# Kernel tuning notes

Hardware: AMD Instinct MI355X
Metric: run time of the kernel (lower is better)

Reference implementation:

```python
import jax, jax.numpy as jnp
import numpy as np
from jax.scipy.linalg import expm

HIDDEN = 1024
STATE = 64
INTER = 4096
EPS = 1e-06
DT_MIN, DT_MAX = 0.001, 0.1


def rmsnorm(x, w, eps=EPS):
    var = jnp.mean(x * x, axis=-1, keepdims=True)
    return x * jax.lax.rsqrt(var + eps) * w


def setup_inputs() -> dict:
    key = jax.random.key(0)
    ks = jax.random.split(key, 10)
    hidden_states = jax.random.normal(ks[0], (4, 2048, HIDDEN), dtype=jnp.float32)
    A = jax.random.normal(ks[1], (STATE, STATE), dtype=jnp.float32) * 0.01
    B = jax.random.normal(ks[2], (STATE, HIDDEN), dtype=jnp.float32) * 0.01
    C = jax.random.normal(ks[3], (HIDDEN, STATE), dtype=jnp.float32) * 0.01
    D = jnp.ones((HIDDEN,), dtype=jnp.float32)
    log_dt = jax.random.uniform(ks[4], (HIDDEN,), dtype=jnp.float32) * (np.log(DT_MAX) - np.log(DT_MIN)) + np.log(DT_MIN)
    s = 1.0 / np.sqrt(HIDDEN)
    w_gate = jax.random.uniform(ks[5], (INTER, HIDDEN), minval=-s, maxval=s, dtype=jnp.float32)
    w_up = jax.random.uniform(ks[6], (INTER, HIDDEN), minval=-s, maxval=s, dtype=jnp.float32)
    s2 = 1.0 / np.sqrt(INTER)
    w_down = jax.random.uniform(ks[7], (HIDDEN, INTER), minval=-s2, maxval=s2, dtype=jnp.float32)
    ln1_w = jnp.ones((HIDDEN,), dtype=jnp.float32)
    ln2_w = jnp.ones((HIDDEN,), dtype=jnp.float32)
    return {"hidden_states": hidden_states, "A": A, "B": B, "C": C, "D": D,
            "log_dt": log_dt, "w_gate": w_gate, "w_up": w_up, "w_down": w_down,
            "ln1_w": ln1_w, "ln2_w": ln2_w}


def ssm(x, A, B, C, D, log_dt):
    # x: (batch, seq, hidden)
    dt = jnp.exp(log_dt)                    # (hidden,)
    A_bar = expm(A * jnp.mean(dt))          # (state, state)
    B_bar = B * dt[None, :]                 # (state, hidden)

    def step(state, x_t):
        # state: (batch, state); x_t: (batch, hidden)
        state = state @ A_bar.T + x_t @ B_bar.T
        out = state @ C.T + D * x_t
        return state, out

    x_t = jnp.swapaxes(x, 0, 1)             # (seq, batch, hidden)
    init = jnp.zeros((x.shape[0], A.shape[0]), dtype=x.dtype)
    _, ys = jax.lax.scan(step, init, x_t)
    return jnp.swapaxes(ys, 0, 1)           # (batch, seq, hidden)


def reference(hidden_states, A, B, C, D, log_dt, w_gate, w_up, w_down, ln1_w, ln2_w):
    # pre-norm SSM mixer + residual
    residual = hidden_states
    h = rmsnorm(hidden_states, ln1_w)
    h = ssm(h, A, B, C, D, log_dt)
    h = residual + h
    # pre-norm SwiGLU FFN + residual
    residual = h
    hn = rmsnorm(h, ln2_w)
    gate = hn @ w_gate.T
    up = hn @ w_up.T
    ffn = (jax.nn.silu(gate) * up) @ w_down.T
    return residual + ffn
```

## Files before the change

kernel.cpp:

```cpp
#include <hip/hip_runtime.h>
#include <hip/hip_bf16.h>
#include <math.h>

typedef __attribute__((ext_vector_type(8))) short short8;
typedef __attribute__((ext_vector_type(4))) float f32x4;
typedef __attribute__((ext_vector_type(4))) int int4v;
typedef __attribute__((ext_vector_type(8))) int int8v;

__device__ __forceinline__ unsigned short f2b(float x) {
  union { float f; unsigned int u; } v; v.f = x;
  unsigned int r = v.u + 0x7fffu + ((v.u >> 16) & 1u);
  return (unsigned short)(r >> 16);
}
__device__ __forceinline__ float b2f(unsigned short u) {
  union { unsigned int u; float f; } v; v.u = ((unsigned int)u) << 16;
  return v.f;
}
__device__ __forceinline__ unsigned char f2f8_sw(float x) {
  float a = fabsf(x);
  unsigned char s = (x < 0.f) ? 0x80 : 0x00;
  if (a >= 464.f) return s | 0x7E;
  union { float f; unsigned u; } v; v.f = a;
  int e = (int)(v.u >> 23) - 127;
  if (e < -6) {
    int q = (int)rintf(a * 512.f);
    if (q >= 8) return s | 0x08;
    return s | (unsigned char)q;
  }
  unsigned mant = v.u & 0x7FFFFF;
  unsigned keep = mant >> 20;
  unsigned rest = mant & 0xFFFFF;
  if (rest > 0x80000u || (rest == 0x80000u && (keep & 1))) keep++;
  unsigned exp8 = (unsigned)(e + 7);
  if (keep == 8) { keep = 0; exp8++; }
  if (exp8 >= 15 && keep >= 7) return s | 0x7E;
  return s | (unsigned char)((exp8 << 3) | keep);
}
#if __has_builtin(__builtin_amdgcn_cvt_pk_fp8_f32)
__device__ __forceinline__ unsigned char f2f8(float x) {
  return (unsigned char)(__builtin_amdgcn_cvt_pk_fp8_f32(x, x, 0, false) & 0xFF);
}
__device__ __forceinline__ unsigned int f8pack4(float a, float b, float c, float d) {
  int w0 = __builtin_amdgcn_cvt_pk_fp8_f32(a, b, 0, false);
  return (unsigned int)__builtin_amdgcn_cvt_pk_fp8_f32(c, d, w0, true);
}
#else
__device__ __forceinline__ unsigned char f2f8(float x) { return f2f8_sw(x); }
__device__ __forceinline__ unsigned int f8pack4(float a, float b, float c, float d) {
  return (unsigned)f2f8_sw(a) | ((unsigned)f2f8_sw(b) << 8) |
         ((unsigned)f2f8_sw(c) << 16) | ((unsigned)f2f8_sw(d) << 24);
}
#endif
__device__ __forceinline__ void async_ld16(const void* g, void* l) {
  __builtin_amdgcn_global_load_lds(
      (const __attribute__((address_space(1))) void*)g,
      (__attribute__((address_space(3))) void*)l, 16, 0, 0);
}

__device__ __forceinline__ f32x4 mx_fp8(int4v alo, int4v ahi, int4v blo, int4v bhi, f32x4 c) {
#if __has_builtin(__builtin_amdgcn_mfma_scale_f32_16x16x128_f8f6f4)
  int8v a = __builtin_shufflevector(alo, ahi, 0, 1, 2, 3, 4, 5, 6, 7);
  int8v b = __builtin_shufflevector(blo, bhi, 0, 1, 2, 3, 4, 5, 6, 7);
  return __builtin_amdgcn_mfma_scale_f32_16x16x128_f8f6f4(
      a, b, c, 0, 0, 0, 0x7F7F7F7F, 0, 0x7F7F7F7F);
#else
  int4v av[2] = {alo, ahi}, bv[2] = {blo, bhi};
  const long* al = (const long*)av;
  const long* bl = (const long*)bv;
#pragma unroll
  for (int j = 0; j < 4; j++)
    c = __builtin_amdgcn_mfma_f32_16x16x32_fp8_fp8(al[j], bl[j], c, 0, 0, 0);
  return c;
#endif
}

__global__ __launch_bounds__(1024) void prep_combo(
    const float* __restrict__ A, const float* __restrict__ logdt,
    float* __restrict__ Abar, float* __restrict__ A64,
    const float* __restrict__ B, const float* __restrict__ Cm,
    unsigned short* __restrict__ Bb, unsigned short* __restrict__ Cb) {
  __shared__ float red[16];
  __shared__ float Ms[4096], T[4096], P[4096];
  if (blockIdx.x != 0) {
    const size_t NB = 65536, NC = 65536;
    size_t base = (size_t)(blockIdx.x - 1) * 1024 + threadIdx.x;
    size_t stride = (size_t)(gridDim.x - 1) * 1024;
    for (size_t id = base; id < NB + NC; id += stride) {
      if (id < NB) { int k = (int)(id & 1023); Bb[id] = f2b(B[id] * expf(logdt[k])); }
      else Cb[id - NB] = f2b(Cm[id - NB]);
    }
    return;
  }
  const int tid = threadIdx.x;
  const int c = tid & 63;
  const int w = tid >> 6;
  float e = expf(logdt[tid]);
#pragma unroll
  for (int off = 32; off > 0; off >>= 1) e += __shfl_down(e, off);
  if (c == 0) red[w] = e;
  __syncthreads();
  if (tid == 0) {
    float s = 0.f;
    for (int i = 0; i < 16; i++) s += red[i];
    red[0] = s * (1.f / 1024.f);
  }
  __syncthreads();
  const float mdt = red[0];
  {
    float m0 = A[tid] * mdt, m1 = A[tid + 1024] * mdt,
          m2 = A[tid + 2048] * mdt, m3 = A[tid + 3072] * mdt;
    Ms[tid] = m0; Ms[tid + 1024] = m1; Ms[tid + 2048] = m2; Ms[tid + 3072] = m3;
    T[tid] = m0; T[tid + 1024] = m1; T[tid + 2048] = m2; T[tid + 3072] = m3;
    P[tid] = m0 + ((tid >> 6) == (tid & 63) ? 1.f : 0.f);
    P[tid + 1024] = m1 + (((tid + 1024) >> 6) == ((tid + 1024) & 63) ? 1.f : 0.f);
    P[tid + 2048] = m2 + (((tid + 2048) >> 6) == ((tid + 2048) & 63) ? 1.f : 0.f);
    P[tid + 3072] = m3 + (((tid + 3072) >> 6) == ((tid + 3072) & 63) ? 1.f : 0.f);
  }
  __syncthreads();
  float colM[64];
#pragma unroll
  for (int j = 0; j < 64; j++) colM[j] = Ms[j * 64 + c];
  for (int k = 2; k <= 6; k++) {
    const float inv = 1.f / (float)k;
    float accs[4];
#pragma unroll
    for (int i = 0; i < 4; i++) {
      const int r = w + 16 * i;
      const float4* Trow = (const float4*)(T + r * 64);
      float a0 = 0.f, a1 = 0.f, a2 = 0.f, a3 = 0.f;
#pragma unroll
      for (int j4 = 0; j4 < 16; j4++) {
        const float4 t = Trow[j4];
        a0 += t.x * colM[4 * j4 + 0]; a1 += t.y * colM[4 * j4 + 1];
        a2 += t.z * colM[4 * j4 + 2]; a3 += t.w * colM[4 * j4 + 3];
      }
      accs[i] = ((a0 + a1) + (a2 + a3)) * inv;
    }
    __syncthreads();
#pragma unroll
    for (int i = 0; i < 4; i++) {
      const int r = w + 16 * i;
      T[r * 64 + c] = accs[i];
      P[r * 64 + c] += accs[i];
    }
    __syncthreads();
  }
#pragma unroll
  for (int i = 0; i < 4; i++) {
    const int r = w + 16 * i;
    Abar[r * 64 + c] = P[r * 64 + c];
    T[r * 64 + c] = P[r * 64 + c];
  }
  __syncthreads();
  for (int sq = 0; sq < 6; sq++) {
    float colT[64];
#pragma unroll
    for (int j = 0; j < 64; j++) colT[j] = T[j * 64 + c];
    float accs[4];
#pragma unroll
    for (int i = 0; i < 4; i++) {
      const int r = w + 16 * i;
      const float4* Trow = (const float4*)(T + r * 64);
      float a0 = 0.f, a1 = 0.f, a2 = 0.f, a3 = 0.f;
#pragma unroll
      for (int j4 = 0; j4 < 16; j4++) {
        const float4 t = Trow[j4];
        a0 += t.x * colT[4 * j4 + 0]; a1 += t.y * colT[4 * j4 + 1];
        a2 += t.z * colT[4 * j4 + 2]; a3 += t.w * colT[4 * j4 + 3];
      }
      accs[i] = (a0 + a1) + (a2 + a3);
    }
    __syncthreads();
#pragma unroll
    for (int i = 0; i < 4; i++) T[(w + 16 * i) * 64 + c] = accs[i];
    __syncthreads();
  }
#pragma unroll
  for (int i = 0; i < 4; i++) {
    const int r = w + 16 * i;
    A64[r * 64 + c] = T[r * 64 + c];
  }
}

__global__ __launch_bounds__(256) void rmsnorm_bf16(
    const float* __restrict__ x, const float* __restrict__ w,
    unsigned short* __restrict__ out) {
  const size_t row = blockIdx.x;
  const int tid = threadIdx.x;
  const float4 v = ((const float4*)(x + row * 1024))[tid];
  float ss = v.x * v.x + v.y * v.y + v.z * v.z + v.w * v.w;
#pragma unroll
  for (int off = 32; off > 0; off >>= 1) ss += __shfl_down(ss, off);
  __shared__ float wsum[4];
  if ((tid & 63) == 0) wsum[tid >> 6] = ss;
  __syncthreads();
  const float tot = wsum[0] + wsum[1] + wsum[2] + wsum[3];
  const float rs = rsqrtf(tot * (1.f / 1024.f) + 1e-6f);
  const float4 wv = ((const float4*)w)[tid];
  ushort4 o;
  o.x = f2b(v.x * rs * wv.x); o.y = f2b(v.y * rs * wv.y);
  o.z = f2b(v.z * rs * wv.z); o.w = f2b(v.w * rs * wv.w);
  ((ushort4*)(out + row * 1024))[tid] = o;
}

__global__ __launch_bounds__(256) void rmsnorm_f8(
    const float* __restrict__ x, const float* __restrict__ w,
    unsigned int* __restrict__ out) {
  const size_t row = blockIdx.x;
  const int tid = threadIdx.x;
  const float4 v = ((const float4*)(x + row * 1024))[tid];
  float ss = v.x * v.x + v.y * v.y + v.z * v.z + v.w * v.w;
#pragma unroll
  for (int off = 32; off > 0; off >>= 1) ss += __shfl_down(ss, off);
  __shared__ float wsum[4];
  if ((tid & 63) == 0) wsum[tid >> 6] = ss;
  __syncthreads();
  const float tot = wsum[0] + wsum[1] + wsum[2] + wsum[3];
  const float rs = rsqrtf(tot * (1.f / 1024.f) + 1e-6f);
  const float4 wv = ((const float4*)w)[tid];
  out[row * 256 + tid] =
      f8pack4(v.x * rs * wv.x, v.y * rs * wv.y, v.z * rs * wv.z, v.w * rs * wv.w);
}

template <int STORE_S>
__global__ __launch_bounds__(256) void scan_combo(
    const float* __restrict__ U, const float* __restrict__ Abar,
    const float* __restrict__ carry, float* __restrict__ zend,
    unsigned short* __restrict__ S,
    const float* __restrict__ csrc, unsigned char* __restrict__ cdst, size_t ccount) {
  constexpr int SCAN_BLOCKS = 32;
  __shared__ float s[4][64];
  if (blockIdx.x >= SCAN_BLOCKS) {
    size_t base = (size_t)(blockIdx.x - SCAN_BLOCKS) * 256 + threadIdx.x;
    size_t stride = (size_t)(gridDim.x - SCAN_BLOCKS) * 256;
    for (size_t id = base; id < ccount; id += stride)
      cdst[id] = f2f8(csrc[id] * 64.f);
    return;
  }
  const int wave = threadIdx.x >> 6, i = threadIdx.x & 63;
  const int task = blockIdx.x * 4 + wave;
  const int b = task >> 5, c = task & 31;
  float a[64];
#pragma unroll
  for (int j = 0; j < 64; j++) a[j] = Abar[i * 64 + j];
  float cur = STORE_S ? carry[(b * 32 + c) * 64 + i] : 0.f;
  const float* Ub = U + ((size_t)(b * 2048 + c * 64)) * 64;
  for (int t = 0; t < 64; t++) {
    s[wave][i] = cur;
    __syncthreads();
    const float u = Ub[t * 64 + i];
    const float4* s4 = (const float4*)s[wave];
    float a0 = u, a1 = 0.f, a2 = 0.f, a3 = 0.f;
#pragma unroll
    for (int j = 0; j < 16; j++) {
      float4 v = s4[j];
      a0 += a[4 * j + 0] * v.x; a1 += a[4 * j + 1] * v.y;
      a2 += a[4 * j + 2] * v.z; a3 += a[4 * j + 3] * v.w;
    }
    cur = (a0 + a1) + (a2 + a3);
    __syncthreads();
    if (STORE_S) S[((size_t)(b * 2048 + c * 64 + t)) * 64 + i] = f2b(cur);
  }
  if (!STORE_S) zend[(b * 32 + c) * 64 + i] = cur;
}

__global__ __launch_bounds__(256) void carry_combo(
    const float* __restrict__ zend, const float* __restrict__ A64,
    float* __restrict__ carry,
    const float* __restrict__ csrc, unsigned char* __restrict__ cdst, size_t ccount) {
  __shared__ float s[4][64];
  if (blockIdx.x != 0) {
    size_t base = (size_t)(blockIdx.x - 1) * 256 + threadIdx.x;
    size_t stride = (size_t)(gridDim.x - 1) * 256;
    for (size_t id = base; id < ccount; id += stride)
      cdst[id] = f2f8(csrc[id] * 64.f);
    return;
  }
  const int b = threadIdx.x >> 6, i = threadIdx.x & 63;
  float a[64];
#pragma unroll
  for (int j = 0; j < 64; j++) a[j] = A64[i * 64 + j];
  float cur = 0.f;
  for (int c = 0; c < 32; c++) {
    carry[(b * 32 + c) * 64 + i] = cur;
    s[b][i] = cur;
    __syncthreads();
    const float z = zend[(b * 32 + c) * 64 + i];
    const float4* s4 = (const float4*)s[b];
    float a0 = z, a1 = 0.f, a2 = 0.f, a3 = 0.f;
#pragma unroll
    for (int j = 0; j < 16; j++) {
      float4 v = s4[j];
      a0 += a[4 * j + 0] * v.x; a1 += a[4 * j + 1] * v.y;
      a2 += a[4 * j + 2] * v.z; a3 += a[4 * j + 3] * v.w;
    }
    cur = (a0 + a1) + (a2 + a3);
    __syncthreads();
  }
}

template <int BM, int BN, int WAVES_M, int WAVES_N, int EPI>
__global__ void __launch_bounds__(256) gemm_bt(
    const unsigned short* __restrict__ X, const unsigned short* __restrict__ W,
    int M, int N, int K,
    float* __restrict__ outf, const unsigned short* __restrict__ e_b,
    const float* __restrict__ e_f, const float* __restrict__ e_d) {
  constexpr int BK = 64;
  constexpr int SM = BM / WAVES_M, SN = BN / WAVES_N;
  constexpr int TM = SM / 16, TN = SN / 16;
  __shared__ unsigned short aT[BM * BK];
  __shared__ unsigned short bT[BN * BK];
  const int tid = threadIdx.x;
  const int lane = tid & 63, wave = tid >> 6;
  const int wm = wave / WAVES_N, wn = wave % WAVES_N;
  const int lm = lane & 15, quad = lane >> 4;
  const long bm0 = (long)blockIdx.y * BM;
  const long bn0 = (long)blockIdx.x * BN;
  const int wb = tid & ~63;

  f32x4 acc[TM][TN];
#pragma unroll
  for (int i = 0; i < TM; i++)
#pragma unroll
    for (int j = 0; j < TN; j++) acc[i][j] = (f32x4){0.f, 0.f, 0.f, 0.f};

  for (int k0 = 0; k0 < K; k0 += BK) {
#pragma unroll
    for (int it = 0; it < (BM * 8) / 256; ++it) {
      int slot = it * 256 + tid;
      int r = slot >> 3, cp = slot & 7, c = cp ^ (r & 7);
      async_ld16(X + (bm0 + r) * (long)K + k0 + c * 8, aT + (it * 256 + wb) * 8);
    }
#pragma unroll
    for (int it = 0; it < (BN * 8) / 256; ++it) {
      int slot = it * 256 + tid;
      int r = slot >> 3, cp = slot & 7, c = cp ^ (r & 7);
      async_ld16(W + (bn0 + r) * (long)K + k0 + c * 8, bT + (it * 256 + wb) * 8);
    }
    __syncthreads();
#pragma unroll
    for (int kk = 0; kk < BK; kk += 32) {
      const int cch = (kk >> 3) + quad;
      short8 af[TM], bf[TN];
#pragma unroll
      for (int i = 0; i < TM; i++) {
        int r = wm * SM + i * 16 + lm;
        af[i] = *(const short8*)(aT + (r * 8 + (cch ^ (r & 7))) * 8);
      }
#pragma unroll
      for (int j = 0; j < TN; j++) {
        int r = wn * SN + j * 16 + lm;
        bf[j] = *(const short8*)(bT + (r * 8 + (cch ^ (r & 7))) * 8);
      }
#pragma unroll
      for (int i = 0; i < TM; i++)
#pragma unroll
        for (int j = 0; j < TN; j++)
          acc[i][j] = __builtin_amdgcn_mfma_f32_16x16x32_bf16(af[i], bf[j], acc[i][j], 0, 0, 0);
    }
    __syncthreads();
  }
#pragma unroll
  for (int i = 0; i < TM; i++) {
#pragma unroll
    for (int j = 0; j < TN; j++) {
#pragma unroll
      for (int r = 0; r < 4; r++) {
        const long m = bm0 + wm * SM + i * 16 + quad * 4 + r;
        const long n = bn0 + wn * SN + j * 16 + lm;
        const long idx = m * N + n;
        const float v = acc[i][j][r];
        if (EPI == 0) outf[idx] = v;
        else if (EPI == 4) outf[idx] = v + e_d[n] * b2f(e_b[idx]) + e_f[idx];
      }
    }
  }
}

__global__ void __launch_bounds__(256) gemm_gu(
    const unsigned char* __restrict__ X, const unsigned char* __restrict__ Wg,
    const unsigned char* __restrict__ Wu, int M, int N, int K,
    unsigned char* __restrict__ out8, float inv) {
  constexpr int BM = 128, BN = 64, BK = 128;
  constexpr int TM = 4, TN = 2;
  __shared__ __attribute__((aligned(16))) unsigned char aT[BM * BK];
  __shared__ __attribute__((aligned(16))) unsigned char gT[BN * BK];
  __shared__ __attribute__((aligned(16))) unsigned char uT[BN * BK];
  const int tid = threadIdx.x;
  const int lane = tid & 63, wave = tid >> 6;
  const int wm = wave >> 1, wn = wave & 1;
  const int lm = lane & 15, quad = lane >> 4;
  const long bm0 = (long)blockIdx.y * BM;
  const long bn0 = (long)blockIdx.x * BN;
  const int wb = tid & ~63;

  f32x4 accg[TM][TN], accu[TM][TN];
#pragma unroll
  for (int i = 0; i < TM; i++)
#pragma unroll
    for (int j = 0; j < TN; j++) {
      accg[i][j] = (f32x4){0.f, 0.f, 0.f, 0.f};
      accu[i][j] = (f32x4){0.f, 0.f, 0.f, 0.f};
    }

  for (int k0 = 0; k0 < K; k0 += BK) {
#pragma unroll
    for (int it = 0; it < 4; ++it) {
      int slot = it * 256 + tid;
      int r = slot >> 3, cp = slot & 7, c = cp ^ (r & 7);
      async_ld16(X + (bm0 + r) * (long)K + k0 + c * 16, aT + (it * 256 + wb) * 16);
    }
#pragma unroll
    for (int it = 0; it < 2; ++it) {
      int slot = it * 256 + tid;
      int r = slot >> 3, cp = slot & 7, c = cp ^ (r & 7);
      async_ld16(Wg + (bn0 + r) * (long)K + k0 + c * 16, gT + (it * 256 + wb) * 16);
    }
#pragma unroll
    for (int it = 0; it < 2; ++it) {
      int slot = it * 256 + tid;
      int r = slot >> 3, cp = slot & 7, c = cp ^ (r & 7);
      async_ld16(Wu + (bn0 + r) * (long)K + k0 + c * 16, uT + (it * 256 + wb) * 16);
    }
    __syncthreads();
    int4v alo[TM], ahi[TM], glo[TN], ghi[TN], ulo[TN], uhi[TN];
#pragma unroll
    for (int i = 0; i < TM; i++) {
      int r = wm * 64 + i * 16 + lm;
      alo[i] = *(const int4v*)(aT + (r * 8 + ((2 * quad) ^ (r & 7))) * 16);
      ahi[i] = *(const int4v*)(aT + (r * 8 + ((2 * quad + 1) ^ (r & 7))) * 16);
    }
#pragma unroll
    for (int j = 0; j < TN; j++) {
      int r = wn * 32 + j * 16 + lm;
      glo[j] = *(const int4v*)(gT + (r * 8 + ((2 * quad) ^ (r & 7))) * 16);
      ghi[j] = *(const int4v*)(gT + (r * 8 + ((2 * quad + 1) ^ (r & 7))) * 16);
      ulo[j] = *(const int4v*)(uT + (r * 8 + ((2 * quad) ^ (r & 7))) * 16);
      uhi[j] = *(const int4v*)(uT + (r * 8 + ((2 * quad + 1) ^ (r & 7))) * 16);
    }
#pragma unroll
    for (int i = 0; i < TM; i++)
#pragma unroll
      for (int j = 0; j < TN; j++) {
        accg[i][j] = mx_fp8(alo[i], ahi[i], glo[j], ghi[j], accg[i][j]);
        accu[i][j] = mx_fp8(alo[i], ahi[i], ulo[j], uhi[j], accu[i][j]);
      }
    __syncthreads();
  }
#pragma unroll
  for (int i = 0; i < TM; i++) {
#pragma unroll
    for (int j = 0; j < TN; j++) {
#pragma unroll
      for (int r = 0; r < 4; r++) {
        const long m = bm0 + wm * 64 + i * 16 + quad * 4 + r;
        const long n = bn0 + wn * 32 + j * 16 + lm;
        const float g = accg[i][j][r] * inv;
        const float u = accu[i][j][r] * inv;
        const float s = g / (1.f + __expf(-g));
        out8[m * N + n] = f2f8(s * u);
      }
    }
  }
}

__global__ void __launch_bounds__(256) gemm_f8(
    const unsigned char* __restrict__ X, const unsigned char* __restrict__ W,
    int M, int N, int K,
    float* __restrict__ outf, const float* __restrict__ e_f, float inv) {
  constexpr int BM = 128, BN = 64, BK = 128;
  constexpr int TM = 4, TN = 2;
  __shared__ __attribute__((aligned(16))) unsigned char aT[BM * BK];
  __shared__ __attribute__((aligned(16))) unsigned char bT[BN * BK];
  const int tid = threadIdx.x;
  const int lane = tid & 63, wave = tid >> 6;
  const int wm = wave >> 1, wn = wave & 1;
  const int lm = lane & 15, quad = lane >> 4;
  const long bm0 = (long)blockIdx.y * BM;
  const long bn0 = (long)blockIdx.x * BN;
  const int wb = tid & ~63;

  f32x4 acc[TM][TN];
#pragma unroll
  for (int i = 0; i < TM; i++)
#pragma unroll
    for (int j = 0; j < TN; j++) acc[i][j] = (f32x4){0.f, 0.f, 0.f, 0.f};

  for (int k0 = 0; k0 < K; k0 += BK) {
#pragma unroll
    for (int it = 0; it < 4; ++it) {
      int slot = it * 256 + tid;
      int r = slot >> 3, cp = slot & 7, c = cp ^ (r & 7);
      async_ld16(X + (bm0 + r) * (long)K + k0 + c * 16, aT + (it * 256 + wb) * 16);
    }
#pragma unroll
    for (int it = 0; it < 2; ++it) {
      int slot = it * 256 + tid;
      int r = slot >> 3, cp = slot & 7, c = cp ^ (r & 7);
      async_ld16(W + (bn0 + r) * (long)K + k0 + c * 16, bT + (it * 256 + wb) * 16);
    }
    __syncthreads();
    int4v alo[TM], ahi[TM], blo[TN], bhi[TN];
#pragma unroll
    for (int i = 0; i < TM; i++) {
      int r = wm * 64 + i * 16 + lm;
      alo[i] = *(const int4v*)(aT + (r * 8 + ((2 * quad) ^ (r & 7))) * 16);
      ahi[i] = *(const int4v*)(aT + (r * 8 + ((2 * quad + 1) ^ (r & 7))) * 16);
    }
#pragma unroll
    for (int j = 0; j < TN; j++) {
      int r = wn * 32 + j * 16 + lm;
      blo[j] = *(const int4v*)(bT + (r * 8 + ((2 * quad) ^ (r & 7))) * 16);
      bhi[j] = *(const int4v*)(bT + (r * 8 + ((2 * quad + 1) ^ (r & 7))) * 16);
    }
#pragma unroll
    for (int i = 0; i < TM; i++)
#pragma unroll
      for (int j = 0; j < TN; j++)
        acc[i][j] = mx_fp8(alo[i], ahi[i], blo[j], bhi[j], acc[i][j]);
    __syncthreads();
  }
#pragma unroll
  for (int i = 0; i < TM; i++) {
#pragma unroll
    for (int j = 0; j < TN; j++) {
#pragma unroll
      for (int r = 0; r < 4; r++) {
        const long m = bm0 + wm * 64 + i * 16 + quad * 4 + r;
        const long n = bn0 + wn * 32 + j * 16 + lm;
        const long idx = m * N + n;
        outf[idx] = acc[i][j][r] * inv + e_f[idx];
      }
    }
  }
}

extern "C" void kernel_launch(void* const* d_in, const int* in_sizes, int n_in,
                              void* d_out, int out_size, void* d_ws, size_t ws_size,
                              hipStream_t stream) {
  const float* x     = (const float*)d_in[0];
  const float* A     = (const float*)d_in[1];
  const float* B     = (const float*)d_in[2];
  const float* C     = (const float*)d_in[3];
  const float* D     = (const float*)d_in[4];
  const float* logdt = (const float*)d_in[5];
  const float* wg    = (const float*)d_in[6];
  const float* wu    = (const float*)d_in[7];
  const float* wd    = (const float*)d_in[8];
  const float* ln1   = (const float*)d_in[9];
  const float* ln2   = (const float*)d_in[10];
  float* out = (float*)d_out;

  char* p = (char*)d_ws;
  auto alloc = [&](size_t bytes) { char* q = p; p += (bytes + 255) & ~(size_t)255; return q; };
  float* Abar  = (float*)alloc(64 * 64 * 4);
  float* A64   = (float*)alloc(64 * 64 * 4);
  float* zend  = (float*)alloc(4 * 32 * 64 * 4);
  float* carry = (float*)alloc(4 * 32 * 64 * 4);
  float* U     = (float*)alloc((size_t)8192 * 64 * 4);
  unsigned short* S    = (unsigned short*)alloc((size_t)8192 * 64 * 2);
  unsigned short* Bb   = (unsigned short*)alloc((size_t)64 * 1024 * 2);
  unsigned short* Cb   = (unsigned short*)alloc((size_t)1024 * 64 * 2);
  unsigned char*  wg8  = (unsigned char*)alloc((size_t)4096 * 1024);
  unsigned char*  wu8  = (unsigned char*)alloc((size_t)4096 * 1024);
  unsigned char*  wd8  = (unsigned char*)alloc((size_t)1024 * 4096);
  unsigned short* xnb  = (unsigned short*)alloc((size_t)8192 * 1024 * 2);
  unsigned char*  hn8  = (unsigned char*)alloc((size_t)8192 * 1024);
  float* h             = (float*)alloc((size_t)8192 * 1024 * 4);
  unsigned char*  act8 = (unsigned char*)alloc((size_t)8192 * 4096);

  const size_t NWG = (size_t)4096 * 1024;

  prep_combo<<<33, 1024, 0, stream>>>(A, logdt, Abar, A64, B, C, Bb, Cb);
  rmsnorm_bf16<<<8192, 256, 0, stream>>>(x, ln1, xnb);
  gemm_bt<32, 64, 2, 2, 0><<<dim3(1, 256), 256, 0, stream>>>(
      xnb, Bb, 8192, 64, 1024, U, nullptr, nullptr, nullptr);
  scan_combo<0><<<32 + 1024, 256, 0, stream>>>(
      U, Abar, nullptr, zend, S, wg, wg8, NWG);
  carry_combo<<<1 + 1024, 256, 0, stream>>>(zend, A64, carry, wu, wu8, NWG);
  scan_combo<1><<<32 + 1024, 256, 0, stream>>>(
      U, Abar, carry, zend, S, wd, wd8, NWG);
  gemm_bt<128, 128, 2, 2, 4><<<dim3(8, 64), 256, 0, stream>>>(
      S, Cb, 8192, 1024, 64, h, xnb, x, D);
  rmsnorm_f8<<<8192, 256, 0, stream>>>(h, ln2, (unsigned int*)hn8);
  gemm_gu<<<dim3(64, 64), 256, 0, stream>>>(
      hn8, wg8, wu8, 8192, 4096, 1024, act8, 1.f / 64.f);
  gemm_f8<<<dim3(16, 64), 256, 0, stream>>>(
      act8, wd8, 8192, 1024, 4096, out, h, 1.f / 64.f);
}
```

Measured before the change: 430.1 us.

## Triple-buffer FP8 FFN GEMMs with async loads and larger 512-thread tiles

Rewrites the gate/up and down-projection FP8 GEMMs to use 512-thread blocks with 256-row tiles (and 128-column tiles for the down projection). The main loop keeps three dynamic-LDS stages, issues async global-to-LDS loads two steps ahead, and waits with explicit vmcnt and raw barriers instead of __syncthreads. LDS reads now fetch 32-byte fragments with a new swizzle, and MFMA issue is wrapped in setprio. The aim is to hide global load latency and raise data reuse per block. The cost is 144KB of LDS per block and fewer blocks, which may limit occupancy or fill the GPU unevenly.

Result: slower. 447.8 us (+4.1%).

```diff
diff --git a/kernel.cpp b/kernel.cpp
--- a/kernel.cpp
+++ b/kernel.cpp
@@ -57,19 +57,19 @@
       (__attribute__((address_space(3))) void*)l, 16, 0, 0);
 }
 
-__device__ __forceinline__ f32x4 mx_fp8(int4v alo, int4v ahi, int4v blo, int4v bhi, f32x4 c) {
+#define VMCNT6()  asm volatile("s_waitcnt vmcnt(6)" ::: "memory")
+#define VMCNT0()  asm volatile("s_waitcnt vmcnt(0)" ::: "memory")
+#define LGKM0()   asm volatile("s_waitcnt lgkmcnt(0)" ::: "memory")
+
+__device__ __forceinline__ f32x4 mx8(int8v a, int8v b, f32x4 c) {
 #if __has_builtin(__builtin_amdgcn_mfma_scale_f32_16x16x128_f8f6f4)
-  int8v a = __builtin_shufflevector(alo, ahi, 0, 1, 2, 3, 4, 5, 6, 7);
-  int8v b = __builtin_shufflevector(blo, bhi, 0, 1, 2, 3, 4, 5, 6, 7);
   return __builtin_amdgcn_mfma_scale_f32_16x16x128_f8f6f4(
       a, b, c, 0, 0, 0, 0x7F7F7F7F, 0, 0x7F7F7F7F);
 #else
-  int4v av[2] = {alo, ahi}, bv[2] = {blo, bhi};
-  const long* al = (const long*)av;
-  const long* bl = (const long*)bv;
+  union { int8v v; long l[4]; } av, bv; av.v = a; bv.v = b;
 #pragma unroll
   for (int j = 0; j < 4; j++)
-    c = __builtin_amdgcn_mfma_f32_16x16x32_fp8_fp8(al[j], bl[j], c, 0, 0, 0);
+    c = __builtin_amdgcn_mfma_f32_16x16x32_fp8_fp8(av.l[j], bv.l[j], c, 0, 0, 0);
   return c;
 #endif
 }
@@ -377,157 +377,199 @@
   }
 }
 
-__global__ void __launch_bounds__(256) gemm_gu(
+
+__global__ void __launch_bounds__(512, 2) gemm_gu2(
     const unsigned char* __restrict__ X, const unsigned char* __restrict__ Wg,
     const unsigned char* __restrict__ Wu, int M, int N, int K,
     unsigned char* __restrict__ out8, float inv) {
-  constexpr int BM = 128, BN = 64, BK = 128;
-  constexpr int TM = 4, TN = 2;
-  __shared__ __attribute__((aligned(16))) unsigned char aT[BM * BK];
-  __shared__ __attribute__((aligned(16))) unsigned char gT[BN * BK];
-  __shared__ __attribute__((aligned(16))) unsigned char uT[BN * BK];
+  extern __shared__ __align__(64) unsigned char smem[];
   const int tid = threadIdx.x;
-  const int lane = tid & 63, wave = tid >> 6;
+  const int lane = tid & 63, wave = tid >> 6, wb = tid & ~63;
   const int wm = wave >> 1, wn = wave & 1;
   const int lm = lane & 15, quad = lane >> 4;
-  const long bm0 = (long)blockIdx.y * BM;
-  const long bn0 = (long)blockIdx.x * BN;
-  const int wb = tid & ~63;
-
-  f32x4 accg[TM][TN], accu[TM][TN];
-#pragma unroll
-  for (int i = 0; i < TM; i++)
-#pragma unroll
-    for (int j = 0; j < TN; j++) {
+  const long bm0 = (long)blockIdx.y * 256;
+  const long bn0 = (long)blockIdx.x * 64;
+  const unsigned char* Xb = X + bm0 * (long)K;
+  const unsigned char* Gb = Wg + bn0 * (long)K;
+  const unsigned char* Ub = Wu + bn0 * (long)K;
+  const int NT = K >> 7;
+
+  f32x4 accg[4][2], accu[4][2];
+#pragma unroll
+  for (int i = 0; i < 4; i++)
+#pragma unroll
+    for (int j = 0; j < 2; j++) {
       accg[i][j] = (f32x4){0.f, 0.f, 0.f, 0.f};
       accu[i][j] = (f32x4){0.f, 0.f, 0.f, 0.f};
     }
 
-  for (int k0 = 0; k0 < K; k0 += BK) {
+  auto stage = [&](int buf, int t) {
+    unsigned char* base = smem + (size_t)buf * 49152;
+    const long k0 = (long)t << 7;
 #pragma unroll
     for (int it = 0; it < 4; ++it) {
-      int slot = it * 256 + tid;
-      int r = slot >> 3, cp = slot & 7, c = cp ^ (r & 7);
-      async_ld16(X + (bm0 + r) * (long)K + k0 + c * 16, aT + (it * 256 + wb) * 16);
-    }
-#pragma unroll
-    for (int it = 0; it < 2; ++it) {
-      int slot = it * 256 + tid;
-      int r = slot >> 3, cp = slot & 7, c = cp ^ (r & 7);
-      async_ld16(Wg + (bn0 + r) * (long)K + k0 + c * 16, gT + (it * 256 + wb) * 16);
-    }
-#pragma unroll
-    for (int it = 0; it < 2; ++it) {
-      int slot = it * 256 + tid;
-      int r = slot >> 3, cp = slot & 7, c = cp ^ (r & 7);
-      async_ld16(Wu + (bn0 + r) * (long)K + k0 + c * 16, uT + (it * 256 + wb) * 16);
-    }
-    __syncthreads();
-    int4v alo[TM], ahi[TM], glo[TN], ghi[TN], ulo[TN], uhi[TN];
-#pragma unroll
-    for (int i = 0; i < TM; i++) {
+      int slot = it * 512 + tid;
+      int r = slot >> 3, cp = slot & 7;
+      int cg = (((cp >> 1) ^ (r & 3)) << 1) | (cp & 1);
+      async_ld16(Xb + (long)r * K + k0 + cg * 16, base + (size_t)(it * 512 + wb) * 16);
+    }
+    {
+      int r = tid >> 3, cp = tid & 7;
+      int cg = (((cp >> 1) ^ (r & 3)) << 1) | (cp & 1);
+      async_ld16(Gb + (long)r * K + k0 + cg * 16, base + 32768 + (size_t)wb * 16);
+      async_ld16(Ub + (long)r * K + k0 + cg * 16, base + 40960 + (size_t)wb * 16);
+    }
+  };
+  auto compute = [&](int buf) {
+    const unsigned char* base = smem + (size_t)buf * 49152;
+    int8v a[4], g[2], u[2];
+#pragma unroll
+    for (int i = 0; i < 4; ++i) {
       int r = wm * 64 + i * 16 + lm;
-      alo[i] = *(const int4v*)(aT + (r * 8 + ((2 * quad) ^ (r & 7))) * 16);
-      ahi[i] = *(const int4v*)(aT + (r * 8 + ((2 * quad + 1) ^ (r & 7))) * 16);
-    }
-#pragma unroll
-    for (int j = 0; j < TN; j++) {
+      a[i] = *(const int8v*)(base + (size_t)((r << 2) + (quad ^ (r & 3))) * 32);
+    }
+#pragma unroll
+    for (int j = 0; j < 2; ++j) {
       int r = wn * 32 + j * 16 + lm;
-      glo[j] = *(const int4v*)(gT + (r * 8 + ((2 * quad) ^ (r & 7))) * 16);
-      ghi[j] = *(const int4v*)(gT + (r * 8 + ((2 * quad + 1) ^ (r & 7))) * 16);
-      ulo[j] = *(const int4v*)(uT + (r * 8 + ((2 * quad) ^ (r & 7))) * 16);
-      uhi[j] = *(const int4v*)(uT + (r * 8 + ((2 * quad + 1) ^ (r & 7))) * 16);
-    }
-#pragma unroll
-    for (int i = 0; i < TM; i++)
-#pragma unroll
-      for (int j = 0; j < TN; j++) {
-        accg[i][j] = mx_fp8(alo[i], ahi[i], glo[j], ghi[j], accg[i][j]);
-        accu[i][j] = mx_fp8(alo[i], ahi[i], ulo[j], uhi[j], accu[i][j]);
-      }
-    __syncthreads();
-  }
-#pragma unroll
-  for (int i = 0; i < TM; i++) {
-#pragma unroll
-    for (int j = 0; j < TN; j++) {
+      size_t off = (size_t)((r << 2) + (quad ^ (r & 3))) * 32;
+      g[j] = *(const int8v*)(base + 32768 + off);
+      u[j] = *(const int8v*)(base + 40960 + off);
+    }
+    __builtin_amdgcn_s_setprio(1);
+#pragma unroll
+    for (int i = 0; i < 4; ++i)
+#pragma unroll
+      for (int j = 0; j < 2; ++j) {
+        accg[i][j] = mx8(a[i], g[j], accg[i][j]);
+        accu[i][j] = mx8(a[i], u[j], accu[i][j]);
+      }
+    __builtin_amdgcn_s_setprio(0);
+  };
+
+  stage(0, 0);
+  stage(1, 1);
+  VMCNT6();
+  __builtin_amdgcn_s_barrier();
+  int bcur = 0;
+  for (int t = 0; t < NT; ++t) {
+    if (t + 2 < NT) {
+      const int bnext = (bcur + 2 >= 3) ? bcur - 1 : bcur + 2;
+      stage(bnext, t + 2);
+    }
+    compute(bcur);
+    if (t + 1 < NT) {
+      LGKM0();
+      if (t + 2 < NT) VMCNT6();
+      else            VMCNT0();
+      __builtin_amdgcn_s_barrier();
+    }
+    bcur = (bcur + 1 == 3) ? 0 : bcur + 1;
+  }
+#pragma unroll
+  for (int i = 0; i < 4; i++) {
+#pragma unroll
+    for (int j = 0; j < 2; j++) {
 #pragma unroll
       for (int r = 0; r < 4; r++) {
         const long m = bm0 + wm * 64 + i * 16 + quad * 4 + r;
         const long n = bn0 + wn * 32 + j * 16 + lm;
-        const float g = accg[i][j][r] * inv;
-        const float u = accu[i][j][r] * inv;
-        const float s = g / (1.f + __expf(-g));
-        out8[m * N + n] = f2f8(s * u);
-      }
-    }
-  }
-}
-
-__global__ void __launch_bounds__(256) gemm_f8(
+        const float gg = accg[i][j][r] * inv;
+        const float uu = accu[i][j][r] * inv;
+        const float s = gg / (1.f + __expf(-gg));
+        out8[m * N + n] = f2f8(s * uu);
+      }
+    }
+  }
+}
+
+__global__ void __launch_bounds__(512, 2) gemm_f82(
     const unsigned char* __restrict__ X, const unsigned char* __restrict__ W,
     int M, int N, int K,
     float* __restrict__ outf, const float* __restrict__ e_f, float inv) {
-  constexpr int BM = 128, BN = 64, BK = 128;
-  constexpr int TM = 4, TN = 2;
-  __shared__ __attribute__((aligned(16))) unsigned char aT[BM * BK];
-  __shared__ __attribute__((aligned(16))) unsigned char bT[BN * BK];
+  extern __shared__ __align__(64) unsigned char smem[];
   const int tid = threadIdx.x;
-  const int lane = tid & 63, wave = tid >> 6;
+  const int lane = tid & 63, wave = tid >> 6, wb = tid & ~63;
   const int wm = wave >> 1, wn = wave & 1;
   const int lm = lane & 15, quad = lane >> 4;
-  const long bm0 = (long)blockIdx.y * BM;
-  const long bn0 = (long)blockIdx.x * BN;
-  const int wb = tid & ~63;
-
-  f32x4 acc[TM][TN];
-#pragma unroll
-  for (int i = 0; i < TM; i++)
-#pragma unroll
-    for (int j = 0; j < TN; j++) acc[i][j] = (f32x4){0.f, 0.f, 0.f, 0.f};
-
-  for (int k0 = 0; k0 < K; k0 += BK) {
+  const long bm0 = (long)blockIdx.y * 256;
+  const long bn0 = (long)blockIdx.x * 128;
+  const unsigned char* Xb = X + bm0 * (long)K;
+  const unsigned char* Wb = W + bn0 * (long)K;
+  const int NT = K >> 7;
+
+  f32x4 acc[4][4];
+#pragma unroll
+  for (int i = 0; i < 4; i++)
+#pragma unroll
+    for (int j = 0; j < 4; j++) acc[i][j] = (f32x4){0.f, 0.f, 0.f, 0.f};
+
+  auto stage = [&](int buf, int t) {
+    unsigned char* base = smem + (size_t)buf * 49152;
+    const long k0 = (long)t << 7;
 #pragma unroll
     for (int it = 0; it < 4; ++it) {
-      int slot = it * 256 + tid;
-      int r = slot >> 3, cp = slot & 7, c = cp ^ (r & 7);
-      async_ld16(X + (bm0 + r) * (long)K + k0 + c * 16, aT + (it * 256 + wb) * 16);
+      int slot = it * 512 + tid;
+      int r = slot >> 3, cp = slot & 7;
+      int cg = (((cp >> 1) ^ (r & 3)) << 1) | (cp & 1);
+      async_ld16(Xb + (long)r * K + k0 + cg * 16, base + (size_t)(it * 512 + wb) * 16);
     }
 #pragma unroll
     for (int it = 0; it < 2; ++it) {
-      int slot = it * 256 + tid;
-      int r = slot >> 3, cp = slot & 7, c = cp ^ (r & 7);
-      async_ld16(W + (bn0 + r) * (long)K + k0 + c * 16, bT + (it * 256 + wb) * 16);
-    }
-    __syncthreads();
-    int4v alo[TM], ahi[TM], blo[TN], bhi[TN];
-#pragma unroll
-    for (int i = 0; i < TM; i++) {
+      int slot = it * 512 + tid;
+      int r = slot >> 3, cp = slot & 7;
+      int cg = (((cp >> 1) ^ (r & 3)) << 1) | (cp & 1);
+      async_ld16(Wb + (long)r * K + k0 + cg * 16, base + 32768 + (size_t)(it * 512 + wb) * 16);
+    }
+  };
+  auto compute = [&](int buf) {
+    const unsigned char* base = smem + (size_t)buf * 49152;
+    int8v a[4], b[4];
+#pragma unroll
+    for (int i = 0; i < 4; ++i) {
       int r = wm * 64 + i * 16 + lm;
-      alo[i] = *(const int4v*)(aT + (r * 8 + ((2 * quad) ^ (r & 7))) * 16);
-      ahi[i] = *(const int4v*)(aT + (r * 8 + ((2 * quad + 1) ^ (r & 7))) * 16);
-    }
-#pragma unroll
-    for (int j = 0; j < TN; j++) {
-      int r = wn * 32 + j * 16 + lm;
-      blo[j] = *(const int4v*)(bT + (r * 8 + ((2 * quad) ^ (r & 7))) * 16);
-      bhi[j] = *(const int4v*)(bT + (r * 8 + ((2 * quad + 1) ^ (r & 7))) * 16);
-    }
-#pragma unroll
-    for (int i = 0; i < TM; i++)
-#pragma unroll
-      for (int j = 0; j < TN; j++)
-        acc[i][j] = mx_fp8(alo[i], ahi[i], blo[j], bhi[j], acc[i][j]);
-    __syncthreads();
-  }
-#pragma unroll
-  for (int i = 0; i < TM; i++) {
-#pragma unroll
-    for (int j = 0; j < TN; j++) {
+      a[i] = *(const int8v*)(base + (size_t)((r << 2) + (quad ^ (r & 3))) * 32);
+    }
+#pragma unroll
+    for (int j = 0; j < 4; ++j) {
+      int r = wn * 64 + j * 16 + lm;
+      b[j] = *(const int8v*)(base + 32768 + (size_t)((r << 2) + (quad ^ (r & 3))) * 32);
+    }
+    __builtin_amdgcn_s_setprio(1);
+#pragma unroll
+    for (int i = 0; i < 4; ++i)
+#pragma unroll
+      for (int j = 0; j < 4; ++j)
+        acc[i][j] = mx8(a[i], b[j], acc[i][j]);
+    __builtin_amdgcn_s_setprio(0);
+  };
+
+  stage(0, 0);
+  stage(1, 1);
+  VMCNT6();
+  __builtin_amdgcn_s_barrier();
+  int bcur = 0;
+  for (int t = 0; t < NT; ++t) {
+    if (t + 2 < NT) {
+      const int bnext = (bcur + 2 >= 3) ? bcur - 1 : bcur + 2;
+      stage(bnext, t + 2);
+    }
+    compute(bcur);
+    if (t + 1 < NT) {
+      LGKM0();
+      if (t + 2 < NT) VMCNT6();
+      else            VMCNT0();
+      __builtin_amdgcn_s_barrier();
+    }
+    bcur = (bcur + 1 == 3) ? 0 : bcur + 1;
+  }
+#pragma unroll
+  for (int i = 0; i < 4; i++) {
+#pragma unroll
+    for (int j = 0; j < 4; j++) {
 #pragma unroll
       for (int r = 0; r < 4; r++) {
         const long m = bm0 + wm * 64 + i * 16 + quad * 4 + r;
-        const long n = bn0 + wn * 32 + j * 16 + lm;
+        const long n = bn0 + wn * 64 + j * 16 + lm;
         const long idx = m * N + n;
         outf[idx] = acc[i][j][r] * inv + e_f[idx];
       }
@@ -570,6 +612,16 @@
   unsigned char*  act8 = (unsigned char*)alloc((size_t)8192 * 4096);
 
   const size_t NWG = (size_t)4096 * 1024;
+  constexpr int DYN_LDS = 3 * 49152;
+
+  static int lds_attr_done = 0;
+  if (!lds_attr_done) {
+    (void)hipFuncSetAttribute((const void*)gemm_gu2,
+                              hipFuncAttributeMaxDynamicSharedMemorySize, DYN_LDS);
+    (void)hipFuncSetAttribute((const void*)gemm_f82,
+                              hipFuncAttributeMaxDynamicSharedMemorySize, DYN_LDS);
+    lds_attr_done = 1;
+  }
 
   prep_combo<<<33, 1024, 0, stream>>>(A, logdt, Abar, A64, B, C, Bb, Cb);
   rmsnorm_bf16<<<8192, 256, 0, stream>>>(x, ln1, xnb);
@@ -583,8 +635,8 @@
   gemm_bt<128, 128, 2, 2, 4><<<dim3(8, 64), 256, 0, stream>>>(
       S, Cb, 8192, 1024, 64, h, xnb, x, D);
   rmsnorm_f8<<<8192, 256, 0, stream>>>(h, ln2, (unsigned int*)hn8);
-  gemm_gu<<<dim3(64, 64), 256, 0, stream>>>(
+  gemm_gu2<<<dim3(64, 32), 512, DYN_LDS, stream>>>(
       hn8, wg8, wu8, 8192, 4096, 1024, act8, 1.f / 64.f);
-  gemm_f8<<<dim3(16, 64), 256, 0, stream>>>(
+  gemm_f82<<<dim3(8, 32), 512, DYN_LDS, stream>>>(
       act8, wd8, 8192, 1024, 4096, out, h, 1.f / 64.f);
 }
```
